# Kernel tuning notes

Hardware: AMD Instinct MI355X
Metric: run time of the kernel (lower is better)

Reference implementation:

```python
import jax, jax.numpy as jnp
import numpy as np

MAX_STEPS = 50
B, H, A = 4096, 1024, 128


def setup_inputs() -> dict:
    key = jax.random.key(0)
    ks = jax.random.split(key, 7)
    s = 1.0 / np.sqrt(H)  # torch default LSTM/Linear init scale
    return {
        "encoder_output": jax.random.normal(ks[0], (1, B, H), dtype=jnp.float32),
        "w_ih": jax.random.normal(ks[1], (4 * H, H), dtype=jnp.float32) * s,
        "w_hh": jax.random.normal(ks[2], (4 * H, H), dtype=jnp.float32) * s,
        "b_ih": jax.random.normal(ks[3], (4 * H,), dtype=jnp.float32) * s,
        "b_hh": jax.random.normal(ks[4], (4 * H,), dtype=jnp.float32) * s,
        "w_pred": jax.random.normal(ks[5], (A, H), dtype=jnp.float32) * s,
        "b_pred": jax.random.normal(ks[6], (A,), dtype=jnp.float32) * s,
    }


def reference(encoder_output, w_ih, w_hh, b_ih, b_hh, w_pred, b_pred):
    # LSTM output (hidden state) of step t; seq_len is always 1.
    hidden = w_hh.shape[1]
    x0 = encoder_output[0]                        # (B, H)
    h0 = jnp.zeros_like(x0)
    c0 = jnp.zeros_like(x0)
    bias = b_ih + b_hh                            # (4H,)

    def step(carry, _):
        x, h, c = carry
        gates = x @ w_ih.T + h @ w_hh.T + bias    # (B, 4H)
        i, f, g, o = jnp.split(gates, 4, axis=-1)  # torch gate order i,f,g,o
        c_new = jax.nn.sigmoid(f) * c + jax.nn.sigmoid(i) * jnp.tanh(g)
        h_new = jax.nn.sigmoid(o) * jnp.tanh(c_new)
        p = h_new @ w_pred.T + b_pred             # (B, A)
        return (h_new, h_new, c_new), p

    _, predicted = jax.lax.scan(step, (x0, h0, c0), None, length=MAX_STEPS)
    return predicted  # (MAX_STEPS, B, A)
```

## Files before the change

kernel.cpp:

```cpp
#include <hip/hip_runtime.h>
#include <hip/hip_bf16.h>
#include <stdint.h>


#define B_SZ   4096
#define H_SZ   1024
#define A_SZ   128
#define NSTEP  50
#define NT     16
#define NTP    8

using bf16 = __hip_bfloat16;
typedef __attribute__((ext_vector_type(8))) short bf16x8;
typedef __attribute__((ext_vector_type(4))) float f32x4;

__device__ __forceinline__ void gload_lds16(const void* g, void* l) {
    __builtin_amdgcn_global_load_lds(
        (const __attribute__((address_space(1))) unsigned int*)g,
        (__attribute__((address_space(3))) unsigned int*)l, 16, 0, 0);
}

#define FENCE() asm volatile("" ::: "memory")
#define BAR()   do { FENCE(); __builtin_amdgcn_s_barrier(); FENCE(); } while (0)
#define VMC6()  asm volatile("s_waitcnt vmcnt(6)" ::: "memory")
#define VMC5()  asm volatile("s_waitcnt vmcnt(5)" ::: "memory")
#define VMC0()  asm volatile("s_waitcnt vmcnt(0)" ::: "memory")
#define LGKM0() asm volatile("s_waitcnt lgkmcnt(0)" ::: "memory")

__device__ __forceinline__ float sigf(float x) {
    return 1.f / (1.f + __expf(-x));
}
__device__ __forceinline__ float tanh_(float x) {
    float e = __expf(-2.f * fabsf(x));
    float t = (1.f - e) / (1.f + e);
    return copysignf(t, x);
}


__global__ void prep_weights(const float4* __restrict__ wih,
                             const float4* __restrict__ whh,
                             bf16* __restrict__ Wc, bf16* __restrict__ Wi) {
    int i = blockIdx.x * 256 + threadIdx.x;
    float4 a = wih[i], b = whh[i];
    bf16 tc[4] = {__float2bfloat16(a.x + b.x), __float2bfloat16(a.y + b.y),
                  __float2bfloat16(a.z + b.z), __float2bfloat16(a.w + b.w)};
    bf16 ti[4] = {__float2bfloat16(a.x), __float2bfloat16(a.y),
                  __float2bfloat16(a.z), __float2bfloat16(a.w)};
    *(uint64_t*)(Wc + 4 * (size_t)i) = *(const uint64_t*)tc;
    *(uint64_t*)(Wi + 4 * (size_t)i) = *(const uint64_t*)ti;
}

__global__ void prep_cast(const float4* __restrict__ in, bf16* __restrict__ out) {
    int i = blockIdx.x * 256 + threadIdx.x;
    float4 a = in[i];
    bf16 t[4] = {__float2bfloat16(a.x), __float2bfloat16(a.y),
                 __float2bfloat16(a.z), __float2bfloat16(a.w)};
    *(uint64_t*)(out + 4 * (size_t)i) = *(const uint64_t*)t;
}

__global__ void prep_bias(const float* __restrict__ a, const float* __restrict__ b,
                          float* __restrict__ o) {
    int i = blockIdx.x * 256 + threadIdx.x;
    o[i] = a[i] + b[i];
}


__global__ __launch_bounds__(512, 2)
void lstm_gates(const bf16* __restrict__ hin, const bf16* __restrict__ W,
                const float* __restrict__ bias, float* __restrict__ c,
                bf16* __restrict__ hout, int step0) {
    __shared__ __align__(16) bf16 sm[65536];
    bf16* const lA0 = sm;
    bf16* const lA1 = sm + 16384;
    bf16* const lB0 = sm + 32768;
    bf16* const lB1 = sm + 49152;

    const int tid    = threadIdx.x;
    const int w      = tid >> 6;
    const int lane   = tid & 63;
    const int wr     = w >> 2;
    const int wc     = w & 3;
    const int lane15 = lane & 15;
    const int lhi    = lane >> 4;

    const int bid     = blockIdx.x;
    const int logical = (bid & 7) * 32 + (bid >> 3);
    const int bm0     = (logical >> 4) * 256;
    const int j0      = (logical & 15) * 64;

    const int scolb = ((tid & 7) * 16) ^ (((tid >> 3) & 7) << 4);
    const char* baseA = (const char*)hin + (size_t)(bm0 + (tid >> 3)) * 2048 + scolb;
    const char* baseB = (const char*)W   + (size_t)(j0  + (tid >> 3)) * 2048 + scolb;

    const int cs0 = ((     lhi * 16) ^ ((lane & 7) << 4)) >> 1;
    const int cs1 = ((64 + lhi * 16) ^ ((lane & 7) << 4)) >> 1;
    const int rA  = (wr * 128 + lane15) * 64;
    const int rB  = (wc * 16  + lane15) * 64;

    f32x4 acc[8][4];
    const f32x4 z = {0.f, 0.f, 0.f, 0.f};
#pragma unroll
    for (int m = 0; m < 8; ++m)
#pragma unroll
        for (int n = 0; n < 4; ++n) acc[m][n] = z;

    auto SGA = [&](int t, int h) {
        bf16* dst = ((t & 1) ? lA1 : lA0) + h * 8192 + w * 512;
        const char* g = baseA + (size_t)(h * 128) * 2048 + (size_t)t * 128;
        gload_lds16(g, dst);
        gload_lds16(g + (size_t)64 * 2048, dst + 4096);
    };
    auto SGB = [&](int t, int h) {
        bf16* dst = ((t & 1) ? lB1 : lB0) + h * 8192 + w * 512;
        const char* g = baseB + (size_t)(h * 2) * 2097152 + (size_t)t * 128;
        gload_lds16(g, dst);
        gload_lds16(g + 2097152, dst + 4096);
    };

    SGB(0, 0); SGB(0, 1); SGA(0, 0); SGA(0, 1);
    SGB(1, 0); SGB(1, 1); SGA(1, 0);

    VMC6();
    BAR();

    for (int t = 0; t < NT; ++t) {
        const bf16* Ad = (t & 1) ? lA1 : lA0;
        const bf16* Bd = (t & 1) ? lB1 : lB0;
        bf16x8 av[4][2], bv[4][2];

#pragma unroll
        for (int m = 0; m < 4; ++m) {
            av[m][0] = *(const bf16x8*)(Ad + rA + m * 1024 + cs0);
            av[m][1] = *(const bf16x8*)(Ad + rA + m * 1024 + cs1);
        }
#pragma unroll
        for (int n = 0; n < 2; ++n) {
            bv[n][0] = *(const bf16x8*)(Bd + rB + n * 4096 + cs0);
            bv[n][1] = *(const bf16x8*)(Bd + rB + n * 4096 + cs1);
        }
        if (t + 1 < NT) SGA(t + 1, 1);
        BAR(); LGKM0();
        __builtin_amdgcn_s_setprio(1);
#pragma unroll
        for (int n = 0; n < 2; ++n)
#pragma unroll
            for (int m = 0; m < 4; ++m) {
                acc[m][n] = __builtin_amdgcn_mfma_f32_16x16x32_bf16(av[m][0], bv[n][0], acc[m][n], 0, 0, 0);
                acc[m][n] = __builtin_amdgcn_mfma_f32_16x16x32_bf16(av[m][1], bv[n][1], acc[m][n], 0, 0, 0);
            }
        __builtin_amdgcn_s_setprio(0);
        BAR();

#pragma unroll
        for (int n = 2; n < 4; ++n) {
            bv[n][0] = *(const bf16x8*)(Bd + rB + n * 4096 + cs0);
            bv[n][1] = *(const bf16x8*)(Bd + rB + n * 4096 + cs1);
        }
        if (t + 2 < NT) SGB(t + 2, 0);
        BAR(); LGKM0();
        __builtin_amdgcn_s_setprio(1);
#pragma unroll
        for (int n = 2; n < 4; ++n)
#pragma unroll
            for (int m = 0; m < 4; ++m) {
                acc[m][n] = __builtin_amdgcn_mfma_f32_16x16x32_bf16(av[m][0], bv[n][0], acc[m][n], 0, 0, 0);
                acc[m][n] = __builtin_amdgcn_mfma_f32_16x16x32_bf16(av[m][1], bv[n][1], acc[m][n], 0, 0, 0);
            }
        __builtin_amdgcn_s_setprio(0);
        BAR();

#pragma unroll
        for (int m = 0; m < 4; ++m) {
            av[m][0] = *(const bf16x8*)(Ad + rA + (m + 4) * 1024 + cs0);
            av[m][1] = *(const bf16x8*)(Ad + rA + (m + 4) * 1024 + cs1);
        }
        if (t + 2 < NT) SGB(t + 2, 1);
        BAR(); LGKM0();
        __builtin_amdgcn_s_setprio(1);
#pragma unroll
        for (int n = 0; n < 2; ++n)
#pragma unroll
            for (int m = 0; m < 4; ++m) {
                acc[m + 4][n] = __builtin_amdgcn_mfma_f32_16x16x32_bf16(av[m][0], bv[n][0], acc[m + 4][n], 0, 0, 0);
                acc[m + 4][n] = __builtin_amdgcn_mfma_f32_16x16x32_bf16(av[m][1], bv[n][1], acc[m + 4][n], 0, 0, 0);
            }
        __builtin_amdgcn_s_setprio(0);
        BAR();

        if (t + 2 < NT) SGA(t + 2, 0);
        BAR(); LGKM0();
        __builtin_amdgcn_s_setprio(1);
#pragma unroll
        for (int n = 2; n < 4; ++n)
#pragma unroll
            for (int m = 0; m < 4; ++m) {
                acc[m + 4][n] = __builtin_amdgcn_mfma_f32_16x16x32_bf16(av[m][0], bv[n][0], acc[m + 4][n], 0, 0, 0);
                acc[m + 4][n] = __builtin_amdgcn_mfma_f32_16x16x32_bf16(av[m][1], bv[n][1], acc[m + 4][n], 0, 0, 0);
            }
        __builtin_amdgcn_s_setprio(0);
        if (t < NT - 1) {
            if (t == NT - 2) { VMC0(); } else { VMC6(); }
        }
        BAR();
    }

    const int jc = j0 + wc * 16 + lane15;
    const float bi  = bias[jc];
    const float bff = bias[H_SZ + jc];
    const float bg  = bias[2 * H_SZ + jc];
    const float bo  = bias[3 * H_SZ + jc];
#pragma unroll
    for (int m = 0; m < 8; ++m) {
#pragma unroll
        for (int r = 0; r < 4; ++r) {
            int row = bm0 + wr * 128 + m * 16 + lhi * 4 + r;
            size_t idx = (size_t)row * H_SZ + jc;
            float iv = acc[m][0][r] + bi;
            float fv = acc[m][1][r] + bff;
            float gv = acc[m][2][r] + bg;
            float ov = acc[m][3][r] + bo;
            float cp = step0 ? 0.f : c[idx];
            float cn = sigf(fv) * cp + sigf(iv) * tanh_(gv);
            float hn = sigf(ov) * tanh_(cn);
            c[idx] = cn;
            hout[idx] = __float2bfloat16(hn);
        }
    }
}


__global__ __launch_bounds__(256)
void pred2(const bf16* __restrict__ h, const bf16* __restrict__ wp,
           const float* __restrict__ bp, float* __restrict__ out) {
    __shared__ __align__(16) bf16 sH[2][2048];
    __shared__ __align__(16) bf16 sP[2][8192];

    const int tid    = threadIdx.x;
    const int w      = tid >> 6;
    const int lane   = tid & 63;
    const int lane15 = lane & 15;
    const int lhi    = lane >> 4;
    const int bm0    = (blockIdx.x >> 1) * 16;
    const int ac0    = (blockIdx.x & 1) * 64;

    const int r   = tid >> 4;
    const int swb = ((tid & 15) * 16) ^ ((r & 7) << 4);
    const char* srcH = (const char*)h  + (size_t)(bm0 + r) * 2048 + swb;
    const char* srcP = (const char*)wp + (size_t)(ac0 + r) * 2048 + swb;

    int eoff[4];
#pragma unroll
    for (int kk = 0; kk < 4; ++kk)
        eoff[kk] = ((kk * 64 + lhi * 16) ^ ((lane15 & 7) << 4)) >> 1;

    f32x4 acc = {0.f, 0.f, 0.f, 0.f};

    auto STAGE = [&](int t) {
        gload_lds16(srcH + (size_t)t * 256, sH[t & 1] + tid * 8);
#pragma unroll
        for (int q = 0; q < 4; ++q)
            gload_lds16(srcP + (size_t)q * 32768 + (size_t)t * 256,
                        sP[t & 1] + q * 2048 + tid * 8);
    };

    STAGE(0);
#pragma unroll
    for (int t = 0; t < NTP; ++t) {
        if (t + 1 < NTP) { STAGE(t + 1); VMC5(); } else { VMC0(); }
        BAR();
        const bf16* Hd = sH[t & 1];
        const bf16* Pd = sP[t & 1];
#pragma unroll
        for (int kk = 0; kk < 4; ++kk) {
            bf16x8 a = *(const bf16x8*)(Hd + lane15 * 128 + eoff[kk]);
            bf16x8 b = *(const bf16x8*)(Pd + (w * 16 + lane15) * 128 + eoff[kk]);
            acc = __builtin_amdgcn_mfma_f32_16x16x32_bf16(a, b, acc, 0, 0, 0);
        }
        BAR();
    }

    const int col = ac0 + w * 16 + lane15;
    const float bpv = bp[col];
#pragma unroll
    for (int rr = 0; rr < 4; ++rr)
        out[(size_t)(bm0 + lhi * 4 + rr) * A_SZ + col] = acc[rr] + bpv;
}


extern "C" void kernel_launch(void* const* d_in, const int* in_sizes, int n_in,
                              void* d_out, int out_size, void* d_ws, size_t ws_size,
                              hipStream_t stream) {
    const float* enc   = (const float*)d_in[0];
    const float* wih   = (const float*)d_in[1];
    const float* whh   = (const float*)d_in[2];
    const float* bih   = (const float*)d_in[3];
    const float* bhh   = (const float*)d_in[4];
    const float* wpred = (const float*)d_in[5];
    const float* bpred = (const float*)d_in[6];
    float* out = (float*)d_out;

    char* ws = (char*)d_ws;
    const size_t WH = (size_t)4 * H_SZ * H_SZ;
    const size_t BH = (size_t)B_SZ * H_SZ;
    bf16*  Wc   = (bf16*)ws;                 ws += WH * 2;
    bf16*  Wi   = (bf16*)ws;                 ws += WH * 2;
    bf16*  h0   = (bf16*)ws;                 ws += BH * 2;
    bf16*  h1   = (bf16*)ws;                 ws += BH * 2;
    float* cbuf = (float*)ws;                ws += BH * 4;
    bf16*  wp   = (bf16*)ws;                 ws += (size_t)A_SZ * H_SZ * 2;
    float* bias = (float*)ws;                ws += 4 * H_SZ * 4;

    prep_weights<<<4096, 256, 0, stream>>>((const float4*)wih, (const float4*)whh, Wc, Wi);
    prep_cast<<<128, 256, 0, stream>>>((const float4*)wpred, wp);
    prep_bias<<<16, 256, 0, stream>>>(bih, bhh, bias);
    prep_cast<<<4096, 256, 0, stream>>>((const float4*)enc, h0);

    bf16* hbuf[2] = {h0, h1};
    for (int s = 0; s < NSTEP; ++s) {
        const bf16* hin = hbuf[s & 1];
        bf16* hout      = hbuf[(s + 1) & 1];
        lstm_gates<<<256, 512, 0, stream>>>(
            hin, (s == 0) ? Wi : Wc, bias, cbuf, hout, s == 0 ? 1 : 0);
        pred2<<<(B_SZ / 16) * 2, 256, 0, stream>>>(
            hout, wp, bpred, out + (size_t)s * (B_SZ * A_SZ));
    }
}
```

Baseline: 2.482 ms.

## Fuse prediction GEMM into next LSTM step kernel as extra blocks

```diff
diff --git a/kernel.cpp b/kernel.cpp
--- a/kernel.cpp
+++ b/kernel.cpp
@@ -65,11 +65,87 @@
 }
 
 
+__device__ __forceinline__ void pred_body(const bf16* __restrict__ h,
+                                          const bf16* __restrict__ wp,
+                                          const float* __restrict__ bp,
+                                          float* __restrict__ pout,
+                                          int pblk, int tid, bf16* sm) {
+    bf16* const pH0 = sm;
+    bf16* const pH1 = sm + 4096;
+    bf16* const pP0 = sm + 8192;
+    bf16* const pP1 = sm + 24576;
+
+    const int w      = tid >> 6;
+    const int lane   = tid & 63;
+    const int lane15 = lane & 15;
+    const int lhi    = lane >> 4;
+    const int bm0    = pblk * 32;
+
+    const int r   = tid >> 4;
+    const int swb = ((tid & 15) * 16) ^ ((r & 7) << 4);
+    const char* srcH = (const char*)h  + (size_t)(bm0 + r) * 2048 + swb;
+    const char* srcP = (const char*)wp + (size_t)r * 2048 + swb;
+
+    int eoff[4];
+#pragma unroll
+    for (int kk = 0; kk < 4; ++kk)
+        eoff[kk] = ((kk * 64 + lhi * 16) ^ ((lane15 & 7) << 4)) >> 1;
+
+    f32x4 acc[2];
+    acc[0] = (f32x4){0.f, 0.f, 0.f, 0.f};
+    acc[1] = (f32x4){0.f, 0.f, 0.f, 0.f};
+
+    auto STAGE = [&](int t) {
+        bf16* dH = ((t & 1) ? pH1 : pH0) + w * 512;
+        bf16* dP = ((t & 1) ? pP1 : pP0) + w * 512;
+        gload_lds16(srcH + (size_t)t * 256, dH);
+#pragma unroll
+        for (int q = 0; q < 4; ++q)
+            gload_lds16(srcP + (size_t)q * 65536 + (size_t)t * 256, dP + q * 4096);
+    };
+
+    STAGE(0);
+#pragma unroll
+    for (int t = 0; t < NTP; ++t) {
+        if (t + 1 < NTP) { STAGE(t + 1); VMC5(); } else { VMC0(); }
+        BAR();
+        const bf16* Hd = (t & 1) ? pH1 : pH0;
+        const bf16* Pd = (t & 1) ? pP1 : pP0;
+#pragma unroll
+        for (int kk = 0; kk < 4; ++kk) {
+            bf16x8 b = *(const bf16x8*)(Pd + (w * 16 + lane15) * 128 + eoff[kk]);
+#pragma unroll
+            for (int m = 0; m < 2; ++m) {
+                bf16x8 a = *(const bf16x8*)(Hd + (m * 16 + lane15) * 128 + eoff[kk]);
+                acc[m] = __builtin_amdgcn_mfma_f32_16x16x32_bf16(a, b, acc[m], 0, 0, 0);
+            }
+        }
+        BAR();
+    }
+
+    const int col = w * 16 + lane15;
+    const float bpv = bp[col];
+#pragma unroll
+    for (int m = 0; m < 2; ++m)
+#pragma unroll
+        for (int rr = 0; rr < 4; ++rr)
+            pout[(size_t)(bm0 + m * 16 + lhi * 4 + rr) * A_SZ + col] = acc[m][rr] + bpv;
+}
+
+
 __global__ __launch_bounds__(512, 2)
-void lstm_gates(const bf16* __restrict__ hin, const bf16* __restrict__ W,
+void lstm_fused(const bf16* __restrict__ hin, const bf16* __restrict__ W,
                 const float* __restrict__ bias, float* __restrict__ c,
-                bf16* __restrict__ hout, int step0) {
+                bf16* __restrict__ hout, int step0,
+                const bf16* __restrict__ wp, const float* __restrict__ bp,
+                float* __restrict__ pout) {
     __shared__ __align__(16) bf16 sm[65536];
+
+    if (blockIdx.x >= 256) {
+        if (pout) pred_body(hin, wp, bp, pout, blockIdx.x - 256, threadIdx.x, sm);
+        return;
+    }
+
     bf16* const lA0 = sm;
     bf16* const lA1 = sm + 16384;
     bf16* const lB0 = sm + 32768;
@@ -229,61 +305,11 @@
 }
 
 
-__global__ __launch_bounds__(256)
-void pred2(const bf16* __restrict__ h, const bf16* __restrict__ wp,
-           const float* __restrict__ bp, float* __restrict__ out) {
-    __shared__ __align__(16) bf16 sH[2][2048];
-    __shared__ __align__(16) bf16 sP[2][8192];
-
-    const int tid    = threadIdx.x;
-    const int w      = tid >> 6;
-    const int lane   = tid & 63;
-    const int lane15 = lane & 15;
-    const int lhi    = lane >> 4;
-    const int bm0    = (blockIdx.x >> 1) * 16;
-    const int ac0    = (blockIdx.x & 1) * 64;
-
-    const int r   = tid >> 4;
-    const int swb = ((tid & 15) * 16) ^ ((r & 7) << 4);
-    const char* srcH = (const char*)h  + (size_t)(bm0 + r) * 2048 + swb;
-    const char* srcP = (const char*)wp + (size_t)(ac0 + r) * 2048 + swb;
-
-    int eoff[4];
-#pragma unroll
-    for (int kk = 0; kk < 4; ++kk)
-        eoff[kk] = ((kk * 64 + lhi * 16) ^ ((lane15 & 7) << 4)) >> 1;
-
-    f32x4 acc = {0.f, 0.f, 0.f, 0.f};
-
-    auto STAGE = [&](int t) {
-        gload_lds16(srcH + (size_t)t * 256, sH[t & 1] + tid * 8);
-#pragma unroll
-        for (int q = 0; q < 4; ++q)
-            gload_lds16(srcP + (size_t)q * 32768 + (size_t)t * 256,
-                        sP[t & 1] + q * 2048 + tid * 8);
-    };
-
-    STAGE(0);
-#pragma unroll
-    for (int t = 0; t < NTP; ++t) {
-        if (t + 1 < NTP) { STAGE(t + 1); VMC5(); } else { VMC0(); }
-        BAR();
-        const bf16* Hd = sH[t & 1];
-        const bf16* Pd = sP[t & 1];
-#pragma unroll
-        for (int kk = 0; kk < 4; ++kk) {
-            bf16x8 a = *(const bf16x8*)(Hd + lane15 * 128 + eoff[kk]);
-            bf16x8 b = *(const bf16x8*)(Pd + (w * 16 + lane15) * 128 + eoff[kk]);
-            acc = __builtin_amdgcn_mfma_f32_16x16x32_bf16(a, b, acc, 0, 0, 0);
-        }
-        BAR();
-    }
-
-    const int col = ac0 + w * 16 + lane15;
-    const float bpv = bp[col];
-#pragma unroll
-    for (int rr = 0; rr < 4; ++rr)
-        out[(size_t)(bm0 + lhi * 4 + rr) * A_SZ + col] = acc[rr] + bpv;
+__global__ __launch_bounds__(512)
+void pred_tail(const bf16* __restrict__ h, const bf16* __restrict__ wp,
+               const float* __restrict__ bp, float* __restrict__ out) {
+    __shared__ __align__(16) bf16 sm2[40960];
+    pred_body(h, wp, bp, out, blockIdx.x, threadIdx.x, sm2);
 }
 
 
@@ -319,9 +345,11 @@
     for (int s = 0; s < NSTEP; ++s) {
         const bf16* hin = hbuf[s & 1];
         bf16* hout      = hbuf[(s + 1) & 1];
-        lstm_gates<<<256, 512, 0, stream>>>(
-            hin, (s == 0) ? Wi : Wc, bias, cbuf, hout, s == 0 ? 1 : 0);
-        pred2<<<(B_SZ / 16) * 2, 256, 0, stream>>>(
-            hout, wp, bpred, out + (size_t)s * (B_SZ * A_SZ));
-    }
-}
+        float* pout = (s == 0) ? nullptr : out + (size_t)(s - 1) * (B_SZ * A_SZ);
+        lstm_fused<<<384, 512, 0, stream>>>(
+            hin, (s == 0) ? Wi : Wc, bias, cbuf, hout, s == 0 ? 1 : 0,
+            wp, bpred, pout);
+    }
+    pred_tail<<<B_SZ / 32, 512, 0, stream>>>(
+        hbuf[0], wp, bpred, out + (size_t)(NSTEP - 1) * (B_SZ * A_SZ));
+}
```

Result: faster. 2.348 ms (-5.4%).
